# Optimization experiments

Hardware: AMD Instinct MI355X
Metric: run time of the kernel (lower is better)

Reference implementation:

```python
import jax, jax.numpy as jnp
import numpy as np

N_ATOMS = 2_000_000
N_MOL = 100_000
ATOMS_PER_MOL = 20
FEAT_DIM = 128
MAX_Z = 86


def setup_inputs() -> dict:
    key = jax.random.key(0)
    k_z, k_f, k_w, k_b = jax.random.split(key, 4)
    z = jax.random.randint(k_z, (N_ATOMS,), 1, MAX_Z)  # avoid padding_idx 0
    f = jax.random.normal(k_f, (N_ATOMS, FEAT_DIM), dtype=jnp.float32)
    num_atoms = jnp.full((N_MOL,), ATOMS_PER_MOL, dtype=jnp.int64)
    w_e = jax.random.normal(k_w, (FEAT_DIM, 1), dtype=jnp.float32) / np.sqrt(FEAT_DIM)
    z_bias = jax.random.normal(k_b, (MAX_Z, 1), dtype=jnp.float32)
    z_bias = z_bias.at[0].set(0.0)  # padding_idx=0 row is zero
    return {"z": z, "f": f, "num_atoms": num_atoms, "w_e": w_e, "z_bias": z_bias}


def reference(z, f, num_atoms, w_e, z_bias):
    n_total = f.shape[0]
    n_mol = num_atoms.shape[0]
    # atomwise energy: linear(feat->1, no bias) + per-element embedding bias
    atomwise = f @ w_e + z_bias[z]  # [N, 1]
    # segment ids: molecule index for each atom (scatter_mol's index tensor)
    seg = jnp.repeat(jnp.arange(n_mol), num_atoms, total_repeat_length=n_total)
    e_total = jax.ops.segment_sum(atomwise, seg, num_segments=n_mol)  # [B, 1]
    return e_total
```

## Files before the change

kernel.cpp:

```cpp
#include <hip/hip_runtime.h>


#define FEAT 128
#define SCAN_CHUNK 1024
#define SCAN_THREADS 256

__global__ void k_partial_sums(const int* __restrict__ cnt, int n,
                               int* __restrict__ block_sums) {
    __shared__ int sdata[SCAN_THREADS];
    const int chunk_base = blockIdx.x * SCAN_CHUNK;
    int local = 0;
    for (int i = threadIdx.x; i < SCAN_CHUNK; i += SCAN_THREADS) {
        int idx = chunk_base + i;
        if (idx < n) local += cnt[idx];
    }
    sdata[threadIdx.x] = local;
    __syncthreads();
    for (int s = SCAN_THREADS / 2; s > 0; s >>= 1) {
        if (threadIdx.x < s) sdata[threadIdx.x] += sdata[threadIdx.x + s];
        __syncthreads();
    }
    if (threadIdx.x == 0) block_sums[blockIdx.x] = sdata[0];
}

__global__ void k_offsets(const int* __restrict__ cnt, int n,
                          const int* __restrict__ block_sums,
                          int* __restrict__ offsets) {
    __shared__ int tsum[SCAN_THREADS];
    __shared__ int s_prefix;
    const int t = threadIdx.x;

    int p = 0;
    for (int j = t; j < blockIdx.x; j += SCAN_THREADS) p += block_sums[j];
    tsum[t] = p;
    __syncthreads();
    for (int s = SCAN_THREADS / 2; s > 0; s >>= 1) {
        if (t < s) tsum[t] += tsum[t + s];
        __syncthreads();
    }
    if (t == 0) s_prefix = tsum[0];
    __syncthreads();
    const int chunk_prefix = s_prefix;
    __syncthreads();

    const int chunk_base = blockIdx.x * SCAN_CHUNK;
    const int per_thread = SCAN_CHUNK / SCAN_THREADS;
    const int base_idx = chunk_base + t * per_thread;

    int v[per_thread];
    int s = 0;
#pragma unroll
    for (int j = 0; j < per_thread; ++j) {
        int idx = base_idx + j;
        v[j] = (idx < n) ? cnt[idx] : 0;
        s += v[j];
    }
    tsum[t] = s;
    __syncthreads();

    for (int off = 1; off < SCAN_THREADS; off <<= 1) {
        int val = (t >= off) ? tsum[t - off] : 0;
        __syncthreads();
        tsum[t] += val;
        __syncthreads();
    }
    int running = chunk_prefix + (tsum[t] - s);
#pragma unroll
    for (int j = 0; j < per_thread; ++j) {
        int idx = base_idx + j;
        if (idx < n) offsets[idx] = running;
        running += v[j];
    }
}

__global__ void __launch_bounds__(256)
k_readout(const float* __restrict__ f, const int* __restrict__ z,
          const int* __restrict__ cnt, const int* __restrict__ offsets,
          const float* __restrict__ w_e, const float* __restrict__ z_bias,
          float* __restrict__ out, int n_mol) {
    __shared__ float s_out[4];
    const int lane = threadIdx.x & 63;
    const int wave = threadIdx.x >> 6;
    const int m = blockIdx.x * 4 + wave;

    if (m < n_mol) {
        const int start = offsets[m];
        const int c = cnt[m];

        const int half = lane >> 5;
        const int qlane = lane & 31;

        const float4 w = reinterpret_cast<const float4*>(w_e)[qlane];

        float acc = 0.f;

        for (int i = lane; i < c; i += 64) acc += z_bias[z[start + i]];

        const float4* __restrict__ f4 = reinterpret_cast<const float4*>(f);
        const int pairs = c >> 1;
        for (int p = 0; p < pairs; ++p) {
            const size_t row = (size_t)(start + 2 * p + half);
            float4 fv = f4[row * (FEAT / 4) + qlane];
            acc = fmaf(fv.x, w.x, acc);
            acc = fmaf(fv.y, w.y, acc);
            acc = fmaf(fv.z, w.z, acc);
            acc = fmaf(fv.w, w.w, acc);
        }
        if ((c & 1) && half == 0) {
            const size_t row = (size_t)(start + c - 1);
            float4 fv = f4[row * (FEAT / 4) + qlane];
            acc = fmaf(fv.x, w.x, acc);
            acc = fmaf(fv.y, w.y, acc);
            acc = fmaf(fv.z, w.z, acc);
            acc = fmaf(fv.w, w.w, acc);
        }

#pragma unroll
        for (int off = 32; off > 0; off >>= 1) acc += __shfl_down(acc, off);
        if (lane == 0) s_out[wave] = acc;
    }
    __syncthreads();

    if (threadIdx.x == 0) {
        const int base = blockIdx.x * 4;
        if (base + 3 < n_mol) {
            float4 v = make_float4(s_out[0], s_out[1], s_out[2], s_out[3]);
            *reinterpret_cast<float4*>(out + base) = v;
        } else {
            for (int i = 0; base + i < n_mol; ++i) out[base + i] = s_out[i];
        }
    }
}

extern "C" void kernel_launch(void* const* d_in, const int* in_sizes, int n_in,
                              void* d_out, int out_size, void* d_ws, size_t ws_size,
                              hipStream_t stream) {
    const int*   z      = (const int*)d_in[0];
    const float* f      = (const float*)d_in[1];
    const int*   cnt    = (const int*)d_in[2];
    const float* w_e    = (const float*)d_in[3];
    const float* z_bias = (const float*)d_in[4];
    float* out = (float*)d_out;

    const int n_mol = in_sizes[2];

    int* offsets    = (int*)d_ws;
    const int nb    = (n_mol + SCAN_CHUNK - 1) / SCAN_CHUNK;
    int* block_sums = offsets + n_mol;

    k_partial_sums<<<nb, SCAN_THREADS, 0, stream>>>(cnt, n_mol, block_sums);
    k_offsets<<<nb, SCAN_THREADS, 0, stream>>>(cnt, n_mol, block_sums, offsets);

    const int waves_per_block = 4;
    const int grid = (n_mol + waves_per_block - 1) / waves_per_block;
    k_readout<<<grid, 256, 0, stream>>>(f, z, cnt, offsets, w_e, z_bias,
                                        out, n_mol);
}
```

Baseline: 181.2 us.

## Fuse scan kernels and add unrolled batched-load path for 20-atom molecules

Drops the separate partial-sum kernel: each scan block now computes its prefix by summing all earlier counts straight from the input, removing one launch at the cost of redundant reads (about 100K ints for the last block). The readout kernel gains a fast path for molecules with exactly 20 atoms that issues five independent float4 loads per lane before the FMAs, raising memory-level parallelism. Other counts fall back to the original loop.

Measured after the change: 238.3 us. 1.32x slower.

```diff
diff --git a/kernel.cpp b/kernel.cpp
--- a/kernel.cpp
+++ b/kernel.cpp
@@ -5,33 +5,15 @@
 #define SCAN_CHUNK 1024
 #define SCAN_THREADS 256
 
-__global__ void k_partial_sums(const int* __restrict__ cnt, int n,
-                               int* __restrict__ block_sums) {
-    __shared__ int sdata[SCAN_THREADS];
-    const int chunk_base = blockIdx.x * SCAN_CHUNK;
-    int local = 0;
-    for (int i = threadIdx.x; i < SCAN_CHUNK; i += SCAN_THREADS) {
-        int idx = chunk_base + i;
-        if (idx < n) local += cnt[idx];
-    }
-    sdata[threadIdx.x] = local;
-    __syncthreads();
-    for (int s = SCAN_THREADS / 2; s > 0; s >>= 1) {
-        if (threadIdx.x < s) sdata[threadIdx.x] += sdata[threadIdx.x + s];
-        __syncthreads();
-    }
-    if (threadIdx.x == 0) block_sums[blockIdx.x] = sdata[0];
-}
-
-__global__ void k_offsets(const int* __restrict__ cnt, int n,
-                          const int* __restrict__ block_sums,
-                          int* __restrict__ offsets) {
+__global__ void k_offsets_fused(const int* __restrict__ cnt, int n,
+                                int* __restrict__ offsets) {
     __shared__ int tsum[SCAN_THREADS];
     __shared__ int s_prefix;
     const int t = threadIdx.x;
+    const int chunk_base = blockIdx.x * SCAN_CHUNK;
 
     int p = 0;
-    for (int j = t; j < blockIdx.x; j += SCAN_THREADS) p += block_sums[j];
+    for (int j = t; j < chunk_base; j += SCAN_THREADS) p += cnt[j];
     tsum[t] = p;
     __syncthreads();
     for (int s = SCAN_THREADS / 2; s > 0; s >>= 1) {
@@ -43,7 +25,6 @@
     const int chunk_prefix = s_prefix;
     __syncthreads();
 
-    const int chunk_base = blockIdx.x * SCAN_CHUNK;
     const int per_thread = SCAN_CHUNK / SCAN_THREADS;
     const int base_idx = chunk_base + t * per_thread;
 
@@ -91,28 +72,47 @@
         const int qlane = lane & 31;
 
         const float4 w = reinterpret_cast<const float4*>(w_e)[qlane];
+        const float4* __restrict__ f4 = reinterpret_cast<const float4*>(f);
 
         float acc = 0.f;
 
         for (int i = lane; i < c; i += 64) acc += z_bias[z[start + i]];
 
-        const float4* __restrict__ f4 = reinterpret_cast<const float4*>(f);
-        const int pairs = c >> 1;
-        for (int p = 0; p < pairs; ++p) {
-            const size_t row = (size_t)(start + 2 * p + half);
-            float4 fv = f4[row * (FEAT / 4) + qlane];
-            acc = fmaf(fv.x, w.x, acc);
-            acc = fmaf(fv.y, w.y, acc);
-            acc = fmaf(fv.z, w.z, acc);
-            acc = fmaf(fv.w, w.w, acc);
-        }
-        if ((c & 1) && half == 0) {
-            const size_t row = (size_t)(start + c - 1);
-            float4 fv = f4[row * (FEAT / 4) + qlane];
-            acc = fmaf(fv.x, w.x, acc);
-            acc = fmaf(fv.y, w.y, acc);
-            acc = fmaf(fv.z, w.z, acc);
-            acc = fmaf(fv.w, w.w, acc);
+        if (c == 20) {
+            const float4* __restrict__ fr =
+                f4 + (size_t)(start + half) * (FEAT / 4) + qlane;
+#pragma unroll
+            for (int h = 0; h < 2; ++h) {
+                float4 v[5];
+#pragma unroll
+                for (int q = 0; q < 5; ++q)
+                    v[q] = fr[(size_t)(h * 5 + q) * (2 * FEAT / 4)];
+#pragma unroll
+                for (int q = 0; q < 5; ++q) {
+                    acc = fmaf(v[q].x, w.x, acc);
+                    acc = fmaf(v[q].y, w.y, acc);
+                    acc = fmaf(v[q].z, w.z, acc);
+                    acc = fmaf(v[q].w, w.w, acc);
+                }
+            }
+        } else {
+            const int pairs = c >> 1;
+            for (int p = 0; p < pairs; ++p) {
+                const size_t row = (size_t)(start + 2 * p + half);
+                float4 fv = f4[row * (FEAT / 4) + qlane];
+                acc = fmaf(fv.x, w.x, acc);
+                acc = fmaf(fv.y, w.y, acc);
+                acc = fmaf(fv.z, w.z, acc);
+                acc = fmaf(fv.w, w.w, acc);
+            }
+            if ((c & 1) && half == 0) {
+                const size_t row = (size_t)(start + c - 1);
+                float4 fv = f4[row * (FEAT / 4) + qlane];
+                acc = fmaf(fv.x, w.x, acc);
+                acc = fmaf(fv.y, w.y, acc);
+                acc = fmaf(fv.z, w.z, acc);
+                acc = fmaf(fv.w, w.w, acc);
+            }
         }
 
 #pragma unroll
@@ -144,12 +144,10 @@
 
     const int n_mol = in_sizes[2];
 
-    int* offsets    = (int*)d_ws;
-    const int nb    = (n_mol + SCAN_CHUNK - 1) / SCAN_CHUNK;
-    int* block_sums = offsets + n_mol;
+    int* offsets = (int*)d_ws;
+    const int nb = (n_mol + SCAN_CHUNK - 1) / SCAN_CHUNK;
 
-    k_partial_sums<<<nb, SCAN_THREADS, 0, stream>>>(cnt, n_mol, block_sums);
-    k_offsets<<<nb, SCAN_THREADS, 0, stream>>>(cnt, n_mol, block_sums, offsets);
+    k_offsets_fused<<<nb, SCAN_THREADS, 0, stream>>>(cnt, n_mol, offsets);
 
     const int waves_per_block = 4;
     const int grid = (n_mol + waves_per_block - 1) / waves_per_block;
```

## Process four molecules per wave with a specialized 20-atom unrolled path

Applied to the files above, without the earlier changes.

Each wave now handles four consecutive molecules rather than one. When all four have exactly 20 atoms, the wave loads the 80 contiguous feature rows in unrolled batches of eight float4 loads, accumulating into four per-molecule registers. The bias gather and the output store are both coalesced across the four molecules. This path is specialized to the test's constant atom count; other counts fall back to a general per-molecule loop. The aim is more memory-level parallelism and fewer blocks, at the cost of more register pressure.

Result: no change. 180.9 us (-0.2%).

```diff
diff --git a/kernel.cpp b/kernel.cpp
--- a/kernel.cpp
+++ b/kernel.cpp
@@ -78,56 +78,94 @@
           const int* __restrict__ cnt, const int* __restrict__ offsets,
           const float* __restrict__ w_e, const float* __restrict__ z_bias,
           float* __restrict__ out, int n_mol) {
-    __shared__ float s_out[4];
-    const int lane = threadIdx.x & 63;
-    const int wave = threadIdx.x >> 6;
-    const int m = blockIdx.x * 4 + wave;
+    const int lane  = threadIdx.x & 63;
+    const int wave  = threadIdx.x >> 6;
+    const int m0    = (blockIdx.x * 4 + wave) * 4;
+    if (m0 >= n_mol) return;
 
-    if (m < n_mol) {
-        const int start = offsets[m];
-        const int c = cnt[m];
+    const int half  = lane >> 5;
+    const int qlane = lane & 31;
 
-        const int half = lane >> 5;
-        const int qlane = lane & 31;
+    const float4 w = reinterpret_cast<const float4*>(w_e)[qlane];
+    const float4* __restrict__ f4 = reinterpret_cast<const float4*>(f);
 
-        const float4 w = reinterpret_cast<const float4*>(w_e)[qlane];
+    bool fast = (m0 + 4 <= n_mol);
+    int c0 = 0, c1 = 0, c2 = 0, c3 = 0;
+    if (fast) {
+        c0 = cnt[m0]; c1 = cnt[m0 + 1]; c2 = cnt[m0 + 2]; c3 = cnt[m0 + 3];
+        fast = (c0 == 20) & (c1 == 20) & (c2 == 20) & (c3 == 20);
+    }
 
-        float acc = 0.f;
+    if (fast) {
+        const int s0 = offsets[m0];
+        float acc0 = 0.f, acc1 = 0.f, acc2 = 0.f, acc3 = 0.f;
 
-        for (int i = lane; i < c; i += 64) acc += z_bias[z[start + i]];
-
-        const float4* __restrict__ f4 = reinterpret_cast<const float4*>(f);
-        const int pairs = c >> 1;
-        for (int p = 0; p < pairs; ++p) {
-            const size_t row = (size_t)(start + 2 * p + half);
-            float4 fv = f4[row * (FEAT / 4) + qlane];
-            acc = fmaf(fv.x, w.x, acc);
-            acc = fmaf(fv.y, w.y, acc);
-            acc = fmaf(fv.z, w.z, acc);
-            acc = fmaf(fv.w, w.w, acc);
-        }
-        if ((c & 1) && half == 0) {
-            const size_t row = (size_t)(start + c - 1);
-            float4 fv = f4[row * (FEAT / 4) + qlane];
-            acc = fmaf(fv.x, w.x, acc);
-            acc = fmaf(fv.y, w.y, acc);
-            acc = fmaf(fv.z, w.z, acc);
-            acc = fmaf(fv.w, w.w, acc);
+        {
+            float b = z_bias[z[s0 + lane]];
+            acc0 += (lane < 20) ? b : 0.f;
+            acc1 += (lane >= 20 && lane < 40) ? b : 0.f;
+            acc2 += (lane >= 40 && lane < 60) ? b : 0.f;
+            acc3 += (lane >= 60) ? b : 0.f;
+            if (lane < 16) acc3 += z_bias[z[s0 + 64 + lane]];
         }
 
+        const float4* __restrict__ fr =
+            f4 + (size_t)(s0 + half) * (FEAT / 4) + qlane;
+#define ACC(p) ((p) < 10 ? acc0 : ((p) < 20 ? acc1 : ((p) < 30 ? acc2 : acc3)))
 #pragma unroll
-        for (int off = 32; off > 0; off >>= 1) acc += __shfl_down(acc, off);
-        if (lane == 0) s_out[wave] = acc;
-    }
-    __syncthreads();
+        for (int b = 0; b < 5; ++b) {
+            float4 v[8];
+#pragma unroll
+            for (int q = 0; q < 8; ++q)
+                v[q] = fr[(size_t)(b * 8 + q) * (2 * FEAT / 4)];
+#pragma unroll
+            for (int q = 0; q < 8; ++q) {
+                const int p = b * 8 + q;
+                float a = ACC(p);
+                a = fmaf(v[q].x, w.x, a);
+                a = fmaf(v[q].y, w.y, a);
+                a = fmaf(v[q].z, w.z, a);
+                a = fmaf(v[q].w, w.w, a);
+                ACC(p) = a;
+            }
+        }
+#undef ACC
 
-    if (threadIdx.x == 0) {
-        const int base = blockIdx.x * 4;
-        if (base + 3 < n_mol) {
-            float4 v = make_float4(s_out[0], s_out[1], s_out[2], s_out[3]);
-            *reinterpret_cast<float4*>(out + base) = v;
-        } else {
-            for (int i = 0; base + i < n_mol; ++i) out[base + i] = s_out[i];
+#pragma unroll
+        for (int off = 32; off > 0; off >>= 1) {
+            acc0 += __shfl_down(acc0, off);
+            acc1 += __shfl_down(acc1, off);
+            acc2 += __shfl_down(acc2, off);
+            acc3 += __shfl_down(acc3, off);
+        }
+        if (lane == 0)
+            *reinterpret_cast<float4*>(out + m0) =
+                make_float4(acc0, acc1, acc2, acc3);
+    } else {
+        for (int k = 0; k < 4 && m0 + k < n_mol; ++k) {
+            const int m = m0 + k;
+            const int start = offsets[m];
+            const int c = cnt[m];
+            float acc = 0.f;
+            for (int i = lane; i < c; i += 64) acc += z_bias[z[start + i]];
+            const int pairs = c >> 1;
+            for (int p = 0; p < pairs; ++p) {
+                float4 fv = f4[(size_t)(start + 2 * p + half) * (FEAT / 4) + qlane];
+                acc = fmaf(fv.x, w.x, acc);
+                acc = fmaf(fv.y, w.y, acc);
+                acc = fmaf(fv.z, w.z, acc);
+                acc = fmaf(fv.w, w.w, acc);
+            }
+            if ((c & 1) && half == 0) {
+                float4 fv = f4[(size_t)(start + c - 1) * (FEAT / 4) + qlane];
+                acc = fmaf(fv.x, w.x, acc);
+                acc = fmaf(fv.y, w.y, acc);
+                acc = fmaf(fv.z, w.z, acc);
+                acc = fmaf(fv.w, w.w, acc);
+            }
+#pragma unroll
+            for (int off = 32; off > 0; off >>= 1) acc += __shfl_down(acc, off);
+            if (lane == 0) out[m] = acc;
         }
     }
 }
@@ -151,8 +189,8 @@
     k_partial_sums<<<nb, SCAN_THREADS, 0, stream>>>(cnt, n_mol, block_sums);
     k_offsets<<<nb, SCAN_THREADS, 0, stream>>>(cnt, n_mol, block_sums, offsets);
 
-    const int waves_per_block = 4;
-    const int grid = (n_mol + waves_per_block - 1) / waves_per_block;
+    const int n_waves = (n_mol + 3) / 4;
+    const int grid    = (n_waves + 3) / 4;
     k_readout<<<grid, 256, 0, stream>>>(f, z, cnt, offsets, w_e, z_bias,
                                         out, n_mol);
 }
```
